# Kernel tuning notes

Measured on AMD Instinct MI355X. Metric: run time of the kernel, lower is better.

The kernel has to match this reference:

```python
import jax, jax.numpy as jnp
import numpy as np

EMBED = 1024
HEADS = 16
HEAD_DIM = EMBED // HEADS


def setup_inputs() -> dict:
    key = jax.random.key(0)
    ks = jax.random.split(key, 11)
    B, L, E = 2, 2048, EMBED
    s = 1.0 / np.sqrt(E)
    return {
        "query": jax.random.normal(ks[0], (B, L, E), jnp.float32),
        "key": jax.random.normal(ks[1], (B, L, E), jnp.float32),
        "value": jax.random.normal(ks[2], (B, L, E), jnp.float32),
        "Wq": jax.random.normal(ks[3], (E, E), jnp.float32) * s,
        "bq": jax.random.normal(ks[4], (E,), jnp.float32) * s,
        "Wk": jax.random.normal(ks[5], (E, E), jnp.float32) * s,
        "bk": jax.random.normal(ks[6], (E,), jnp.float32) * s,
        "Wv": jax.random.normal(ks[7], (E, E), jnp.float32) * s,
        "bv": jax.random.normal(ks[8], (E,), jnp.float32) * s,
        "Wo": jax.random.normal(ks[9], (E, E), jnp.float32) * s,
        "bo": jax.random.normal(ks[10], (E,), jnp.float32) * s,
    }


def reference(query, key, value, Wq, bq, Wk, bk, Wv, bv, Wo, bo):
    B, Lq, E = query.shape
    Lk = key.shape[1]
    # Linear projections (torch Linear: x @ W.T + b)
    q = (query @ Wq.T + bq).reshape(B, Lq, HEADS, HEAD_DIM).transpose(0, 2, 1, 3)
    k = (key @ Wk.T + bk).reshape(B, Lk, HEADS, HEAD_DIM).transpose(0, 2, 1, 3)
    v = (value @ Wv.T + bv).reshape(B, Lk, HEADS, HEAD_DIM).transpose(0, 2, 1, 3)
    # NOTE: original scales by sqrt(embed_size), not sqrt(head_dim)
    energy = jnp.einsum("bhqd,bhkd->bhqk", q, k) / jnp.sqrt(jnp.float32(E))
    attn = jax.nn.softmax(energy, axis=-1)
    out = jnp.einsum("bhqk,bhkd->bhqd", attn, v)  # [B,H,Lq,D]
    out = out.transpose(0, 2, 1, 3).reshape(B, Lq, E)
    return out @ Wo.T + bo
```

## Files before the change

### kernel.cpp

```cpp
#include <hip/hip_runtime.h>
#include <hip/hip_bf16.h>


typedef __attribute__((ext_vector_type(4))) float f32x4;
typedef __attribute__((ext_vector_type(16))) float f32x16;
typedef __attribute__((ext_vector_type(8))) short bf16x8;
typedef __attribute__((ext_vector_type(4))) short bf16x4;
typedef __attribute__((ext_vector_type(2))) unsigned int u32x2;

static __device__ __forceinline__ unsigned short f2bf(float f) {
  union { float f; unsigned int u; } a; a.f = f;
  unsigned int u = a.u;
  u += 0x7FFFu + ((u >> 16) & 1u);
  return (unsigned short)(u >> 16);
}

static __device__ __forceinline__ unsigned pack2(float lo, float hi) {
  unsigned a = __float_as_uint(lo) + 0x8000u;
  unsigned b = __float_as_uint(hi) + 0x8000u;
  return __builtin_amdgcn_perm(b, a, 0x07060302);
}

#define AS1(p) ((const __attribute__((address_space(1))) void*)(p))
#define AS3(p) ((__attribute__((address_space(3))) void*)(p))

__global__ __launch_bounds__(256) void cvt_kernel(
    const float* __restrict__ q, const float* __restrict__ k, const float* __restrict__ v,
    const float* __restrict__ wq, const float* __restrict__ wk, const float* __restrict__ wv,
    const float* __restrict__ wo, short* __restrict__ ws) {
  long i = (long)blockIdx.x * 256 + threadIdx.x;
  long e = i * 8;
  const float* src; long off;
  if (e < 12582912) {
    int s = (int)(e >> 22);
    src = s == 0 ? q : (s == 1 ? k : v);
    off = e & 4194303;
  } else {
    long e2 = e - 12582912;
    int s = (int)(e2 >> 20);
    src = s == 0 ? wq : (s == 1 ? wk : (s == 2 ? wv : wo));
    off = e2 & 1048575;
  }
  f32x4 a = *(const f32x4*)(src + off);
  f32x4 b = *(const f32x4*)(src + off + 4);
  bf16x8 o;
  o[0] = (short)f2bf(a[0]); o[1] = (short)f2bf(a[1]);
  o[2] = (short)f2bf(a[2]); o[3] = (short)f2bf(a[3]);
  o[4] = (short)f2bf(b[0]); o[5] = (short)f2bf(b[1]);
  o[6] = (short)f2bf(b[2]); o[7] = (short)f2bf(b[3]);
  *(bf16x8*)(ws + e) = o;
}

__device__ __forceinline__ void gemm_tile(const short* __restrict__ A, const short* __restrict__ B,
                                          int m0, int n0, f32x4 acc[4][4],
                                          short* As, short* Bs) {
  const int t = threadIdx.x;
  const int lane = t & 63, w = t >> 6;
  const int wr = w >> 1, wc = w & 1;
  const int x = lane & 15, g = lane >> 4;
  const int ar = lane >> 2, ac = (lane & 3) * 8;

#pragma unroll
  for (int fm = 0; fm < 4; fm++)
#pragma unroll
    for (int fn = 0; fn < 4; fn++)
#pragma unroll
      for (int r = 0; r < 4; r++) acc[fm][fn][r] = 0.0f;

  for (int k0 = 0; k0 < 1024; k0 += 32) {
    __syncthreads();
#pragma unroll
    for (int i = 0; i < 2; i++) {
      int ch = w * 2 + i;
      const short* ga = A + (long)(m0 + ch * 16 + ar) * 1024 + k0 + ac;
      __builtin_amdgcn_global_load_lds(AS1(ga), AS3(As + ch * 512), 16, 0, 0);
      const short* gb = B + (long)(n0 + ch * 16 + ar) * 1024 + k0 + ac;
      __builtin_amdgcn_global_load_lds(AS1(gb), AS3(Bs + ch * 512), 16, 0, 0);
    }
    __syncthreads();
    bf16x8 af[4], bfv[4];
#pragma unroll
    for (int f = 0; f < 4; f++) {
      af[f]  = *(const bf16x8*)(As + (wr * 64 + f * 16 + x) * 32 + g * 8);
      bfv[f] = *(const bf16x8*)(Bs + (wc * 64 + f * 16 + x) * 32 + g * 8);
    }
#pragma unroll
    for (int fm = 0; fm < 4; fm++)
#pragma unroll
      for (int fn = 0; fn < 4; fn++)
        acc[fm][fn] = __builtin_amdgcn_mfma_f32_16x16x32_bf16(af[fm], bfv[fn], acc[fm][fn], 0, 0, 0);
  }
}

__global__ __launch_bounds__(256) void proj_kernel(
    const short* __restrict__ Xq, const short* __restrict__ Xk, const short* __restrict__ Xv,
    const short* __restrict__ Wq, const short* __restrict__ Wk, const short* __restrict__ Wv,
    const float* __restrict__ bq, const float* __restrict__ bk, const float* __restrict__ bv,
    short* __restrict__ Qo, short* __restrict__ Ko, short* __restrict__ Vto) {
  __shared__ short As[4096], Bs[4096];
  const int z = blockIdx.z;
  const short* A = z == 0 ? Xq : (z == 1 ? Xk : Xv);
  const short* B = z == 0 ? Wq : (z == 1 ? Wk : Wv);
  const float* bias = z == 0 ? bq : (z == 1 ? bk : bv);
  const int m0 = blockIdx.y * 128, n0 = blockIdx.x * 128;
  f32x4 acc[4][4];
  gemm_tile(A, B, m0, n0, acc, As, Bs);

  const int lane = threadIdx.x & 63, w = threadIdx.x >> 6;
  const int wr = w >> 1, wc = w & 1, x = lane & 15, g = lane >> 4;

  if (z == 0) {
    const float scale = 0.04508422002778f;
#pragma unroll
    for (int fn = 0; fn < 4; fn++) {
      int n = n0 + wc * 64 + fn * 16 + x;
      float bb = bias[n];
      int h = n >> 6, d = n & 63;
#pragma unroll
      for (int fm = 0; fm < 4; fm++) {
        int mb = m0 + wr * 64 + fm * 16 + g * 4;
#pragma unroll
        for (int r = 0; r < 4; r++) {
          int m = mb + r;
          int b = m >> 11, l = m & 2047;
          float val = (acc[fm][fn][r] + bb) * scale;
          Qo[((long)((b * 16 + h) * 2048 + l)) * 64 + d] = (short)f2bf(val);
        }
      }
    }
  } else if (z == 1) {
#pragma unroll
    for (int fn = 0; fn < 4; fn++) {
      int n = n0 + wc * 64 + fn * 16 + x;
      float bb = bias[n];
      int h = n >> 6, d = n & 63;
#pragma unroll
      for (int fm = 0; fm < 4; fm++) {
        int mb = m0 + wr * 64 + fm * 16 + g * 4;
#pragma unroll
        for (int r = 0; r < 4; r++) {
          int m = mb + r;
          int b = m >> 11, kv = m & 2047;
          int ds = d ^ ((kv & 7) << 3);
          Ko[((long)((b * 16 + h) * 2048 + kv)) * 64 + ds] = (short)f2bf(acc[fm][fn][r] + bb);
        }
      }
    }
  } else {
#pragma unroll
    for (int fn = 0; fn < 4; fn++) {
      int n = n0 + wc * 64 + fn * 16 + x;
      float bb = bias[n];
      int h = n >> 6, d = n & 63;
#pragma unroll
      for (int fm = 0; fm < 4; fm++) {
        int mb = m0 + wr * 64 + fm * 16 + g * 4;
        int b = mb >> 11, kvb = mb & 2047;
        bf16x4 pk;
#pragma unroll
        for (int r = 0; r < 4; r++) pk[r] = (short)f2bf(acc[fm][fn][r] + bb);
        int kvs = (kvb & ~63) | ((kvb & 63) ^ ((d & 7) << 3));
        *(bf16x4*)(Vto + ((long)((b * 16 + h) * 64 + d)) * 2048 + kvs) = pk;
      }
    }
  }
}

__global__ __launch_bounds__(256, 2) void attn_kernel(
    const short* __restrict__ Qg, const short* __restrict__ Kg,
    const short* __restrict__ Vtg, short* __restrict__ Og) {
  __shared__ __align__(16) short Kl[2][4096];
  __shared__ __align__(16) short Vl[2][4096];
  __shared__ __align__(16) short Pl[4][32][64];
  const int t = threadIdx.x, w = t >> 6, lane = t & 63;
  const int col = lane & 31, hi = lane >> 5;
  const int bh = blockIdx.y;
  const int q0 = blockIdx.x * 128 + w * 32;
  const long hb = (long)bh * 2048 * 64;
  const int swz = (col & 7) * 8;

  bf16x8 qf[4];
#pragma unroll
  for (int ksl = 0; ksl < 4; ksl++)
    qf[ksl] = *(const bf16x8*)(Qg + hb + (long)(q0 + col) * 64 + ksl * 16 + hi * 8);

  f32x16 o0, o1;
#pragma unroll
  for (int i = 0; i < 16; i++) { o0[i] = 0.0f; o1[i] = 0.0f; }
  float l_r = 0.0f;

  auto stage = [&](int buf, int kv0) {
#pragma unroll
    for (int it = 0; it < 2; it++) {
      int cb = it * 256 + w * 64;
      const short* gk = Kg + hb + (long)kv0 * 64 + (cb + lane) * 8;
      __builtin_amdgcn_global_load_lds(AS1(gk), AS3(&Kl[buf][cb * 8]), 16, 0, 0);
      int c = cb + lane;
      const short* gv = Vtg + hb + (long)(c >> 3) * 2048 + kv0 + (c & 7) * 8;
      __builtin_amdgcn_global_load_lds(AS1(gv), AS3(&Vl[buf][cb * 8]), 16, 0, 0);
    }
  };

  stage(0, 0);
  __syncthreads();

  for (int ti = 0; ti < 32; ti++) {
    const int buf = ti & 1;
    if (ti < 31) stage(buf ^ 1, (ti + 1) * 64);

    f32x16 s0, s1;
#pragma unroll
    for (int i = 0; i < 16; i++) { s0[i] = 0.0f; s1[i] = 0.0f; }
    __builtin_amdgcn_s_setprio(1);
#pragma unroll
    for (int ksl = 0; ksl < 4; ksl++) {
      int dcol = (ksl * 16 + hi * 8) ^ swz;
      bf16x8 a0 = *(const bf16x8*)(&Kl[buf][col * 64 + dcol]);
      bf16x8 a1 = *(const bf16x8*)(&Kl[buf][(col + 32) * 64 + dcol]);
      s0 = __builtin_amdgcn_mfma_f32_32x32x16_bf16(a0, qf[ksl], s0, 0, 0, 0);
      s1 = __builtin_amdgcn_mfma_f32_32x32x16_bf16(a1, qf[ksl], s1, 0, 0, 0);
    }
    __builtin_amdgcn_s_setprio(0);

#pragma unroll
    for (int i = 0; i < 16; i++) { s0[i] = __builtin_amdgcn_exp2f(s0[i]); }
#pragma unroll
    for (int i = 0; i < 16; i++) { s1[i] = __builtin_amdgcn_exp2f(s1[i]); }
    {
      float a0 = s0[0] + s0[1], a1 = s0[2] + s0[3], a2 = s0[4] + s0[5], a3 = s0[6] + s0[7];
      float a4 = s0[8] + s0[9], a5 = s0[10] + s0[11], a6 = s0[12] + s0[13], a7 = s0[14] + s0[15];
      float b0 = s1[0] + s1[1], b1 = s1[2] + s1[3], b2 = s1[4] + s1[5], b3 = s1[6] + s1[7];
      float b4 = s1[8] + s1[9], b5 = s1[10] + s1[11], b6 = s1[12] + s1[13], b7 = s1[14] + s1[15];
      float c0 = a0 + a1, c1 = a2 + a3, c2 = a4 + a5, c3 = a6 + a7;
      float c4 = b0 + b1, c5 = b2 + b3, c6 = b4 + b5, c7 = b6 + b7;
      float d0 = c0 + c1, d1 = c2 + c3, d2 = c4 + c5, d3 = c6 + c7;
      l_r += (d0 + d1) + (d2 + d3);
    }

#pragma unroll
    for (int j = 0; j < 4; j++) {
      u32x2 p0, p1;
      p0[0] = pack2(s0[4 * j + 0], s0[4 * j + 1]);
      p0[1] = pack2(s0[4 * j + 2], s0[4 * j + 3]);
      int kv = 8 * j + 4 * hi;
      *(u32x2*)&Pl[w][col][kv ^ swz] = p0;
      p1[0] = pack2(s1[4 * j + 0], s1[4 * j + 1]);
      p1[1] = pack2(s1[4 * j + 2], s1[4 * j + 3]);
      *(u32x2*)&Pl[w][col][(32 + kv) ^ swz] = p1;
    }

    __builtin_amdgcn_s_setprio(1);
#pragma unroll
    for (int KS = 0; KS < 4; KS++) {
      const int vcol = (KS * 16 + hi * 8) ^ swz;
      bf16x8 pb  = *(const bf16x8*)&Pl[w][col][vcol];
      bf16x8 vb0 = *(const bf16x8*)(&Vl[buf][col * 64 + vcol]);
      bf16x8 vb1 = *(const bf16x8*)(&Vl[buf][(col + 32) * 64 + vcol]);
      o0 = __builtin_amdgcn_mfma_f32_32x32x16_bf16(vb0, pb, o0, 0, 0, 0);
      o1 = __builtin_amdgcn_mfma_f32_32x32x16_bf16(vb1, pb, o1, 0, 0, 0);
    }
    __builtin_amdgcn_s_setprio(0);

    __syncthreads();
  }

  const float l_tot = l_r + __shfl_xor(l_r, 32);
  const float inv = 1.0f / l_tot;
  const int b = bh >> 4, h = bh & 15;
  const long base = ((long)(b * 2048 + q0 + col) * 16 + h) * 64;
#pragma unroll
  for (int dh = 0; dh < 2; dh++) {
#pragma unroll
    for (int g2 = 0; g2 < 4; g2++) {
      float x0 = (dh ? o1[g2 * 4 + 0] : o0[g2 * 4 + 0]) * inv;
      float x1 = (dh ? o1[g2 * 4 + 1] : o0[g2 * 4 + 1]) * inv;
      float x2 = (dh ? o1[g2 * 4 + 2] : o0[g2 * 4 + 2]) * inv;
      float x3 = (dh ? o1[g2 * 4 + 3] : o0[g2 * 4 + 3]) * inv;
      u32x2 rr;
      rr[0] = (unsigned)f2bf(x0) | ((unsigned)f2bf(x1) << 16);
      rr[1] = (unsigned)f2bf(x2) | ((unsigned)f2bf(x3) << 16);
      int d = dh * 32 + g2 * 8 + hi * 4;
      *(u32x2*)(Og + base + d) = rr;
    }
  }
}

__global__ __launch_bounds__(256) void out_kernel(
    const short* __restrict__ O, const short* __restrict__ Wo,
    const float* __restrict__ bo, float* __restrict__ out) {
  __shared__ short As[4096], Bs[4096];
  const int m0 = blockIdx.y * 128, n0 = blockIdx.x * 128;
  f32x4 acc[4][4];
  gemm_tile(O, Wo, m0, n0, acc, As, Bs);
  const int lane = threadIdx.x & 63, w = threadIdx.x >> 6;
  const int wr = w >> 1, wc = w & 1, x = lane & 15, g = lane >> 4;
#pragma unroll
  for (int fn = 0; fn < 4; fn++) {
    int n = n0 + wc * 64 + fn * 16 + x;
    float bb = bo[n];
#pragma unroll
    for (int fm = 0; fm < 4; fm++) {
      int mb = m0 + wr * 64 + fm * 16 + g * 4;
#pragma unroll
      for (int r = 0; r < 4; r++)
        out[(long)(mb + r) * 1024 + n] = acc[fm][fn][r] + bb;
    }
  }
}

extern "C" void kernel_launch(void* const* d_in, const int* in_sizes, int n_in,
                              void* d_out, int out_size, void* d_ws, size_t ws_size,
                              hipStream_t stream) {
  const float* q  = (const float*)d_in[0];
  const float* k  = (const float*)d_in[1];
  const float* v  = (const float*)d_in[2];
  const float* wq = (const float*)d_in[3];
  const float* bq = (const float*)d_in[4];
  const float* wk = (const float*)d_in[5];
  const float* bk = (const float*)d_in[6];
  const float* wv = (const float*)d_in[7];
  const float* bv = (const float*)d_in[8];
  const float* wo = (const float*)d_in[9];
  const float* bo = (const float*)d_in[10];

  short* ws  = (short*)d_ws;
  short* Xq  = ws;
  short* Xk  = Xq + 4194304;
  short* Xv  = Xk + 4194304;
  short* Wqb = Xv + 4194304;
  short* Wkb = Wqb + 1048576;
  short* Wvb = Wkb + 1048576;
  short* Wob = Wvb + 1048576;
  short* Qb  = Wob + 1048576;
  short* Kb  = Qb + 4194304;
  short* Vtb = Kb + 4194304;
  short* Ob  = Vtb + 4194304;

  cvt_kernel<<<8192, 256, 0, stream>>>(q, k, v, wq, wk, wv, wo, ws);
  dim3 gp(8, 32, 3);
  proj_kernel<<<gp, 256, 0, stream>>>(Xq, Xk, Xv, Wqb, Wkb, Wvb, bq, bk, bv, Qb, Kb, Vtb);
  dim3 ga(16, 32);
  attn_kernel<<<ga, 256, 0, stream>>>(Qb, Kb, Vtb, Ob);
  dim3 gf(8, 32);
  out_kernel<<<gf, 256, 0, stream>>>(Ob, Wob, bo, (float*)d_out);
}
```

Before: 144.1 us.

## Fuse activation bf16 conversion into projection GEMM and pass P via shuffles

The separate conversion pass over the fp32 query/key/value activations is removed. The projection GEMM now loads fp32 A tiles directly, packs them to bf16 in registers and stores them to LDS, so only the weights are still converted up front. In the attention kernel, the P matrix no longer round-trips through an LDS buffer: each lane packs its own bf16 values and swaps the other half with its partner lane via a cross-lane shuffle to build the MFMA operand. This saves a full read/write of the activations and LDS traffic, but the GEMM A loads become synchronous register loads instead of direct global-to-LDS loads, and the attention kernel adds shuffle instructions.

```diff
diff --git a/kernel.cpp b/kernel.cpp
--- a/kernel.cpp
+++ b/kernel.cpp
@@ -24,23 +24,15 @@
 #define AS1(p) ((const __attribute__((address_space(1))) void*)(p))
 #define AS3(p) ((__attribute__((address_space(3))) void*)(p))
 
-__global__ __launch_bounds__(256) void cvt_kernel(
-    const float* __restrict__ q, const float* __restrict__ k, const float* __restrict__ v,
-    const float* __restrict__ wq, const float* __restrict__ wk, const float* __restrict__ wv,
-    const float* __restrict__ wo, short* __restrict__ ws) {
+__global__ __launch_bounds__(256) void cvtw_kernel(
+    const float* __restrict__ wq, const float* __restrict__ wk,
+    const float* __restrict__ wv, const float* __restrict__ wo,
+    short* __restrict__ ws) {
   long i = (long)blockIdx.x * 256 + threadIdx.x;
   long e = i * 8;
-  const float* src; long off;
-  if (e < 12582912) {
-    int s = (int)(e >> 22);
-    src = s == 0 ? q : (s == 1 ? k : v);
-    off = e & 4194303;
-  } else {
-    long e2 = e - 12582912;
-    int s = (int)(e2 >> 20);
-    src = s == 0 ? wq : (s == 1 ? wk : (s == 2 ? wv : wo));
-    off = e2 & 1048575;
-  }
+  int s = (int)(e >> 20);
+  const float* src = s == 0 ? wq : (s == 1 ? wk : (s == 2 ? wv : wo));
+  long off = e & 1048575;
   f32x4 a = *(const f32x4*)(src + off);
   f32x4 b = *(const f32x4*)(src + off + 4);
   bf16x8 o;
@@ -51,6 +43,59 @@
   *(bf16x8*)(ws + e) = o;
 }
 
+__device__ __forceinline__ void gemm_tile_f32a(const float* __restrict__ A,
+                                               const short* __restrict__ B,
+                                               int m0, int n0, f32x4 acc[4][4],
+                                               short* As, short* Bs) {
+  const int t = threadIdx.x;
+  const int lane = t & 63, w = t >> 6;
+  const int wr = w >> 1, wc = w & 1;
+  const int x = lane & 15, g = lane >> 4;
+  const int ar = lane >> 2, ac = (lane & 3) * 8;
+
+#pragma unroll
+  for (int fm = 0; fm < 4; fm++)
+#pragma unroll
+    for (int fn = 0; fn < 4; fn++)
+#pragma unroll
+      for (int r = 0; r < 4; r++) acc[fm][fn][r] = 0.0f;
+
+  for (int k0 = 0; k0 < 1024; k0 += 32) {
+    __syncthreads();
+#pragma unroll
+    for (int i = 0; i < 2; i++) {
+      int ch = w * 2 + i;
+      const short* gb = B + (long)(n0 + ch * 16 + ar) * 1024 + k0 + ac;
+      __builtin_amdgcn_global_load_lds(AS1(gb), AS3(Bs + ch * 512), 16, 0, 0);
+    }
+#pragma unroll
+    for (int i = 0; i < 2; i++) {
+      int ch = w * 2 + i;
+      const float* ga = A + (long)(m0 + ch * 16 + ar) * 1024 + k0 + ac;
+      f32x4 a = *(const f32x4*)ga;
+      f32x4 b = *(const f32x4*)(ga + 4);
+      union { unsigned u[4]; bf16x8 v; } pk;
+      pk.u[0] = pack2(a[0], a[1]);
+      pk.u[1] = pack2(a[2], a[3]);
+      pk.u[2] = pack2(b[0], b[1]);
+      pk.u[3] = pack2(b[2], b[3]);
+      *(bf16x8*)(As + ch * 512 + lane * 8) = pk.v;
+    }
+    __syncthreads();
+    bf16x8 af[4], bfv[4];
+#pragma unroll
+    for (int f = 0; f < 4; f++) {
+      af[f]  = *(const bf16x8*)(As + (wr * 64 + f * 16 + x) * 32 + g * 8);
+      bfv[f] = *(const bf16x8*)(Bs + (wc * 64 + f * 16 + x) * 32 + g * 8);
+    }
+#pragma unroll
+    for (int fm = 0; fm < 4; fm++)
+#pragma unroll
+      for (int fn = 0; fn < 4; fn++)
+        acc[fm][fn] = __builtin_amdgcn_mfma_f32_16x16x32_bf16(af[fm], bfv[fn], acc[fm][fn], 0, 0, 0);
+  }
+}
+
 __device__ __forceinline__ void gemm_tile(const short* __restrict__ A, const short* __restrict__ B,
                                           int m0, int n0, f32x4 acc[4][4],
                                           short* As, short* Bs) {
@@ -93,18 +138,18 @@
 }
 
 __global__ __launch_bounds__(256) void proj_kernel(
-    const short* __restrict__ Xq, const short* __restrict__ Xk, const short* __restrict__ Xv,
+    const float* __restrict__ Xq, const float* __restrict__ Xk, const float* __restrict__ Xv,
     const short* __restrict__ Wq, const short* __restrict__ Wk, const short* __restrict__ Wv,
     const float* __restrict__ bq, const float* __restrict__ bk, const float* __restrict__ bv,
     short* __restrict__ Qo, short* __restrict__ Ko, short* __restrict__ Vto) {
   __shared__ short As[4096], Bs[4096];
   const int z = blockIdx.z;
-  const short* A = z == 0 ? Xq : (z == 1 ? Xk : Xv);
+  const float* A = z == 0 ? Xq : (z == 1 ? Xk : Xv);
   const short* B = z == 0 ? Wq : (z == 1 ? Wk : Wv);
   const float* bias = z == 0 ? bq : (z == 1 ? bk : bv);
   const int m0 = blockIdx.y * 128, n0 = blockIdx.x * 128;
   f32x4 acc[4][4];
-  gemm_tile(A, B, m0, n0, acc, As, Bs);
+  gemm_tile_f32a(A, B, m0, n0, acc, As, Bs);
 
   const int lane = threadIdx.x & 63, w = threadIdx.x >> 6;
   const int wr = w >> 1, wc = w & 1, x = lane & 15, g = lane >> 4;
@@ -171,7 +216,6 @@
     const short* __restrict__ Vtg, short* __restrict__ Og) {
   __shared__ __align__(16) short Kl[2][4096];
   __shared__ __align__(16) short Vl[2][4096];
-  __shared__ __align__(16) short Pl[4][32][64];
   const int t = threadIdx.x, w = t >> 6, lane = t & 63;
   const int col = lane & 31, hi = lane >> 5;
   const int bh = blockIdx.y;
@@ -237,29 +281,32 @@
       l_r += (d0 + d1) + (d2 + d3);
     }
 
-#pragma unroll
-    for (int j = 0; j < 4; j++) {
-      u32x2 p0, p1;
-      p0[0] = pack2(s0[4 * j + 0], s0[4 * j + 1]);
-      p0[1] = pack2(s0[4 * j + 2], s0[4 * j + 3]);
-      int kv = 8 * j + 4 * hi;
-      *(u32x2*)&Pl[w][col][kv ^ swz] = p0;
-      p1[0] = pack2(s1[4 * j + 0], s1[4 * j + 1]);
-      p1[1] = pack2(s1[4 * j + 2], s1[4 * j + 3]);
-      *(u32x2*)&Pl[w][col][(32 + kv) ^ swz] = p1;
-    }
-
-    __builtin_amdgcn_s_setprio(1);
-#pragma unroll
-    for (int KS = 0; KS < 4; KS++) {
-      const int vcol = (KS * 16 + hi * 8) ^ swz;
-      bf16x8 pb  = *(const bf16x8*)&Pl[w][col][vcol];
-      bf16x8 vb0 = *(const bf16x8*)(&Vl[buf][col * 64 + vcol]);
-      bf16x8 vb1 = *(const bf16x8*)(&Vl[buf][(col + 32) * 64 + vcol]);
-      o0 = __builtin_amdgcn_mfma_f32_32x32x16_bf16(vb0, pb, o0, 0, 0, 0);
-      o1 = __builtin_amdgcn_mfma_f32_32x32x16_bf16(vb1, pb, o1, 0, 0, 0);
-    }
-    __builtin_amdgcn_s_setprio(0);
+#define PVSTEP(SEL, KS)                                                       \
+    {                                                                         \
+      const int qo = 4 * (((KS) & 1) * 2 + hi);                               \
+      const int qx = 4 * (((KS) & 1) * 2 + (hi ^ 1));                         \
+      unsigned own0 = pack2(SEL[qo + 0], SEL[qo + 1]);                        \
+      unsigned own1 = pack2(SEL[qo + 2], SEL[qo + 3]);                        \
+      unsigned out0 = pack2(SEL[qx + 0], SEL[qx + 1]);                        \
+      unsigned out1 = pack2(SEL[qx + 2], SEL[qx + 3]);                        \
+      unsigned r0 = __shfl_xor(out0, 32);                                     \
+      unsigned r1 = __shfl_xor(out1, 32);                                     \
+      union { unsigned u[4]; bf16x8 v; } pb;                                  \
+      pb.u[0] = hi ? r0 : own0; pb.u[1] = hi ? r1 : own1;                     \
+      pb.u[2] = hi ? own0 : r0; pb.u[3] = hi ? own1 : r1;                     \
+      const int vcol = ((KS) * 16 + hi * 8) ^ swz;                            \
+      bf16x8 vb0 = *(const bf16x8*)(&Vl[buf][col * 64 + vcol]);               \
+      bf16x8 vb1 = *(const bf16x8*)(&Vl[buf][(col + 32) * 64 + vcol]);        \
+      __builtin_amdgcn_s_setprio(1);                                          \
+      o0 = __builtin_amdgcn_mfma_f32_32x32x16_bf16(vb0, pb.v, o0, 0, 0, 0);   \
+      o1 = __builtin_amdgcn_mfma_f32_32x32x16_bf16(vb1, pb.v, o1, 0, 0, 0);   \
+      __builtin_amdgcn_s_setprio(0);                                          \
+    }
+    PVSTEP(s0, 0)
+    PVSTEP(s0, 1)
+    PVSTEP(s1, 2)
+    PVSTEP(s1, 3)
+#undef PVSTEP
 
     __syncthreads();
   }
@@ -324,10 +371,7 @@
   const float* bo = (const float*)d_in[10];
 
   short* ws  = (short*)d_ws;
-  short* Xq  = ws;
-  short* Xk  = Xq + 4194304;
-  short* Xv  = Xk + 4194304;
-  short* Wqb = Xv + 4194304;
+  short* Wqb = ws;
   short* Wkb = Wqb + 1048576;
   short* Wvb = Wkb + 1048576;
   short* Wob = Wvb + 1048576;
@@ -336,9 +380,9 @@
   short* Vtb = Kb + 4194304;
   short* Ob  = Vtb + 4194304;
 
-  cvt_kernel<<<8192, 256, 0, stream>>>(q, k, v, wq, wk, wv, wo, ws);
+  cvtw_kernel<<<2048, 256, 0, stream>>>(wq, wk, wv, wo, ws);
   dim3 gp(8, 32, 3);
-  proj_kernel<<<gp, 256, 0, stream>>>(Xq, Xk, Xv, Wqb, Wkb, Wvb, bq, bk, bv, Qb, Kb, Vtb);
+  proj_kernel<<<gp, 256, 0, stream>>>(q, k, v, Wqb, Wkb, Wvb, bq, bk, bv, Qb, Kb, Vtb);
   dim3 ga(16, 32);
   attn_kernel<<<ga, 256, 0, stream>>>(Qb, Kb, Vtb, Ob);
   dim3 gf(8, 32);
```

New measurement: 338.3 us. 135% more time.
